# Kernel optimization log

Hardware: AMD Instinct MI355X
Metric: run time of the kernel (lower is better)

## Reference

```python
import jax, jax.numpy as jnp
import numpy as np

GROUP_SIZE = 128

def setup_inputs() -> dict:
    key = jax.random.key(0)
    k1, k2, k3, k4 = jax.random.split(key, 4)
    in_f, out_f = 4096, 4096
    num_groups = (in_f + GROUP_SIZE - 1) // GROUP_SIZE  # 32
    x = jax.random.normal(k1, (4, 2048, in_f), dtype=jnp.float32)
    qweight = jax.random.randint(k2, (out_f, in_f), 0, 16, dtype=jnp.int32)
    scales = jax.random.uniform(k3, (out_f, num_groups), dtype=jnp.float32)
    bias = jax.random.normal(k4, (out_f,), dtype=jnp.float32)
    return {"x": x, "qweight": qweight, "scales": scales, "bias": bias}

def reference(x, qweight, scales, bias):
    out_f, in_f = qweight.shape
    # group-wise dequantize: broadcast each per-group scale over its columns
    scale_full = jnp.repeat(scales, GROUP_SIZE, axis=1)[:, :in_f]  # [out, in]
    weight = qweight.astype(scales.dtype) * scale_full             # [out, in]
    # F.linear(x, weight, bias) == x @ weight.T + bias
    return jnp.einsum('bsi,oi->bso', x, weight) + bias
```

## Files before the change

### kernel.cpp

```cpp
#include <hip/hip_runtime.h>
#include <hip/hip_bf16.h>

typedef __bf16 bf16_t;
typedef __bf16 bf16x8 __attribute__((ext_vector_type(8)));
typedef float  f32x4  __attribute__((ext_vector_type(4)));

static constexpr int M_ = 8192;
static constexpr int N_ = 4096;
static constexpr int K_ = 4096;

static constexpr int BM = 256, BN = 256, BK = 64;
static constexpr int NT = K_ / BK;
static constexpr int HT_ELEMS  = 128 * 64;
static constexpr int BUF_ELEMS = 2 * HT_ELEMS;

__device__ __forceinline__ void load_lds16(const bf16_t* g, bf16_t* l) {
  __builtin_amdgcn_global_load_lds(
      (const __attribute__((address_space(1))) void*)g,
      (__attribute__((address_space(3))) void*)l,
      16, 0, 0);
}

#define MFMA16(a, b, c) __builtin_amdgcn_mfma_f32_16x16x32_bf16((a), (b), (c), 0, 0, 0)

__global__ __launch_bounds__(256) void cvt_x_kernel(const float* __restrict__ x,
                                                    bf16_t* __restrict__ xb) {
  const size_t i = ((size_t)blockIdx.x * 256 + threadIdx.x) * 8;
  const float4 f0 = *(const float4*)(x + i);
  const float4 f1 = *(const float4*)(x + i + 4);
  bf16x8 o;
  o[0] = (bf16_t)f0.x; o[1] = (bf16_t)f0.y; o[2] = (bf16_t)f0.z; o[3] = (bf16_t)f0.w;
  o[4] = (bf16_t)f1.x; o[5] = (bf16_t)f1.y; o[6] = (bf16_t)f1.z; o[7] = (bf16_t)f1.w;
  *(bf16x8*)(xb + i) = o;
}

__global__ __launch_bounds__(256) void dequant_kernel(const int* __restrict__ q,
                                                      const float* __restrict__ s,
                                                      bf16_t* __restrict__ wb) {
  const size_t base = ((size_t)blockIdx.x * 256 + threadIdx.x) * 8;
  const int o  = (int)(base >> 12);
  const int ii = (int)(base & 4095);
  const float sc = s[(o << 5) + (ii >> 7)];
  const int4 q0 = *(const int4*)(q + base);
  const int4 q1 = *(const int4*)(q + base + 4);
  bf16x8 w;
  w[0] = (bf16_t)((float)q0.x * sc); w[1] = (bf16_t)((float)q0.y * sc);
  w[2] = (bf16_t)((float)q0.z * sc); w[3] = (bf16_t)((float)q0.w * sc);
  w[4] = (bf16_t)((float)q1.x * sc); w[5] = (bf16_t)((float)q1.y * sc);
  w[6] = (bf16_t)((float)q1.z * sc); w[7] = (bf16_t)((float)q1.w * sc);
  *(bf16x8*)(wb + base) = w;
}

__global__ __launch_bounds__(512, 2) void gemm_kernel(const bf16_t* __restrict__ A,
                                                      const bf16_t* __restrict__ B,
                                                      const float* __restrict__ bias,
                                                      float* __restrict__ C) {
  __shared__ __align__(16) bf16_t As[2 * BUF_ELEMS];
  __shared__ __align__(16) bf16_t Bs[2 * BUF_ELEMS];

  const int tid  = threadIdx.x;
  const int lane = tid & 63;
  const int wave = tid >> 6;
  const int ln = lane & 15;
  const int lq = lane >> 4;
  const int wm = wave >> 2;
  const int wn = wave & 3;

  const int bid = blockIdx.x;
  const int wg  = (bid & 7) * 64 + (bid >> 3);
  const int bn  = (wg & 15) * BN;
  const int bm  = (wg >> 4) * BM;

  const int r_sub = tid >> 3;
  const int g_col = ((tid & 7) ^ (r_sub & 7)) * 8;
  const size_t a_base = (size_t)(bm + r_sub) * K_ + g_col;
  const size_t b_base = (size_t)(bn + r_sub) * K_ + g_col;
  const int lds_off = tid * 8;

  auto stageA = [&](int t, int h) {
    bf16_t* d = As + (t & 1) * BUF_ELEMS + h * HT_ELEMS + lds_off;
    const bf16_t* s = A + a_base + (size_t)(h * 128) * K_ + (size_t)t * BK;
    load_lds16(s, d);
    load_lds16(s + (size_t)64 * K_, d + 4096);
  };
  auto stageB = [&](int t, int h) {
    bf16_t* d = Bs + (t & 1) * BUF_ELEMS + h * HT_ELEMS + lds_off;
    const bf16_t* s = B + b_base + (size_t)(h * 128) * K_ + (size_t)t * BK;
    load_lds16(s, d);
    load_lds16(s + (size_t)64 * K_, d + 4096);
  };

  const int kx0 = (lq * 8) ^ ((ln & 7) * 8);
  const int kx1 = (32 + lq * 8) ^ ((ln & 7) * 8);
  const int a_row_off = (wm * 16 + ln) * 64;
  const int b_row_off = (wn * 32 + ln) * 64;

  f32x4 acc[8][4] = {};

  stageA(0, 0); stageB(0, 0); stageB(0, 1); stageA(0, 1);
  stageA(1, 0); stageB(1, 0); stageB(1, 1);
  asm volatile("s_waitcnt vmcnt(6)" ::: "memory");
  __builtin_amdgcn_s_barrier();

  for (int T = 0; T < NT; ++T) {
    const bf16_t* as = As + (T & 1) * BUF_ELEMS;
    const bf16_t* bs = Bs + (T & 1) * BUF_ELEMS;
    bf16x8 af[4][2], bqA[2][2], bqB[2][2];

#pragma unroll
    for (int i = 0; i < 4; ++i) {
      const bf16_t* p = as + a_row_off + i * 2048;
      af[i][0] = *(const bf16x8*)(p + kx0);
      af[i][1] = *(const bf16x8*)(p + kx1);
    }
#pragma unroll
    for (int j = 0; j < 2; ++j) {
      const bf16_t* p = bs + b_row_off + j * 1024;
      bqA[j][0] = *(const bf16x8*)(p + kx0);
      bqA[j][1] = *(const bf16x8*)(p + kx1);
    }
    if (T + 1 < NT) stageA(T + 1, 1);
    asm volatile("s_waitcnt lgkmcnt(8)" ::: "memory");
    __builtin_amdgcn_s_barrier();
    asm volatile("s_waitcnt lgkmcnt(0)" ::: "memory");
    __builtin_amdgcn_sched_barrier(0);
    __builtin_amdgcn_s_setprio(1);
#pragma unroll
    for (int i = 0; i < 4; ++i)
#pragma unroll
      for (int j = 0; j < 2; ++j) {
        acc[i][j] = MFMA16(af[i][0], bqA[j][0], acc[i][j]);
        acc[i][j] = MFMA16(af[i][1], bqA[j][1], acc[i][j]);
      }
    __builtin_amdgcn_s_setprio(0);
    __builtin_amdgcn_s_barrier();

#pragma unroll
    for (int j = 0; j < 2; ++j) {
      const bf16_t* p = bs + HT_ELEMS + b_row_off + j * 1024;
      bqB[j][0] = *(const bf16x8*)(p + kx0);
      bqB[j][1] = *(const bf16x8*)(p + kx1);
    }
    if (T + 2 < NT) stageA(T + 2, 0);
    __builtin_amdgcn_s_barrier();
    asm volatile("s_waitcnt lgkmcnt(0)" ::: "memory");
    __builtin_amdgcn_sched_barrier(0);
    __builtin_amdgcn_s_setprio(1);
#pragma unroll
    for (int i = 0; i < 4; ++i)
#pragma unroll
      for (int j = 0; j < 2; ++j) {
        acc[i][j + 2] = MFMA16(af[i][0], bqB[j][0], acc[i][j + 2]);
        acc[i][j + 2] = MFMA16(af[i][1], bqB[j][1], acc[i][j + 2]);
      }
    __builtin_amdgcn_s_setprio(0);
    __builtin_amdgcn_s_barrier();

#pragma unroll
    for (int i = 0; i < 4; ++i) {
      const bf16_t* p = as + HT_ELEMS + a_row_off + i * 2048;
      af[i][0] = *(const bf16x8*)(p + kx0);
      af[i][1] = *(const bf16x8*)(p + kx1);
    }
    if (T + 2 < NT) stageB(T + 2, 0);
    __builtin_amdgcn_s_barrier();
    asm volatile("s_waitcnt lgkmcnt(0)" ::: "memory");
    __builtin_amdgcn_sched_barrier(0);
    __builtin_amdgcn_s_setprio(1);
#pragma unroll
    for (int i = 0; i < 4; ++i)
#pragma unroll
      for (int j = 0; j < 2; ++j) {
        acc[i + 4][j + 2] = MFMA16(af[i][0], bqB[j][0], acc[i + 4][j + 2]);
        acc[i + 4][j + 2] = MFMA16(af[i][1], bqB[j][1], acc[i + 4][j + 2]);
      }
    __builtin_amdgcn_s_setprio(0);
    __builtin_amdgcn_s_barrier();

    if (T + 2 < NT) {
      stageB(T + 2, 1);
      asm volatile("s_waitcnt vmcnt(6)" ::: "memory");
    } else {
      asm volatile("s_waitcnt vmcnt(0)" ::: "memory");
    }
    __builtin_amdgcn_s_barrier();
    __builtin_amdgcn_sched_barrier(0);
    __builtin_amdgcn_s_setprio(1);
#pragma unroll
    for (int i = 0; i < 4; ++i)
#pragma unroll
      for (int j = 0; j < 2; ++j) {
        acc[i + 4][j] = MFMA16(af[i][0], bqA[j][0], acc[i + 4][j]);
        acc[i + 4][j] = MFMA16(af[i][1], bqA[j][1], acc[i + 4][j]);
      }
    __builtin_amdgcn_s_setprio(0);
    __builtin_amdgcn_s_barrier();
  }

#pragma unroll
  for (int j = 0; j < 4; ++j) {
    const int col = bn + (j >> 1) * 128 + wn * 32 + (j & 1) * 16 + ln;
    const float bv = bias[col];
#pragma unroll
    for (int i = 0; i < 8; ++i) {
      const int row0 = bm + (i >> 2) * 128 + (i & 3) * 32 + wm * 16 + lq * 4;
      float* cp = C + (size_t)row0 * N_ + col;
#pragma unroll
      for (int r = 0; r < 4; ++r) {
        *cp = acc[i][j][r] + bv;
        cp += N_;
      }
    }
  }
}

extern "C" void kernel_launch(void* const* d_in, const int* in_sizes, int n_in,
                              void* d_out, int out_size, void* d_ws, size_t ws_size,
                              hipStream_t stream) {
  const float* x    = (const float*)d_in[0];
  const int*   qw   = (const int*)d_in[1];
  const float* sc   = (const float*)d_in[2];
  const float* bias = (const float*)d_in[3];
  float* out = (float*)d_out;

  bf16_t* xb = (bf16_t*)d_ws;
  bf16_t* wb = xb + (size_t)M_ * K_;

  cvt_x_kernel<<<(int)(((size_t)M_ * K_) / (256 * 8)), 256, 0, stream>>>(x, xb);
  dequant_kernel<<<(int)(((size_t)N_ * K_) / (256 * 8)), 256, 0, stream>>>(qw, sc, wb);

  const int nwg = (N_ / BN) * (M_ / BM);
  gemm_kernel<<<nwg, 512, 0, stream>>>(xb, wb, bias, out);
}
```

Baseline: 491.3 us.

## Prefetch next tile's B fragments during last phase and stage epilogue through LDS

```diff
diff --git a/kernel.cpp b/kernel.cpp
--- a/kernel.cpp
+++ b/kernel.cpp
@@ -96,120 +96,160 @@
   const int b_row_off = (wn * 32 + ln) * 64;
 
   f32x4 acc[8][4] = {};
+  bf16x8 bq0[2][2], bq1[2][2];
+
+#define TILE_BODY(T_, AS_, BS_, BQC_, BQN_)                                    \
+  {                                                                            \
+    const bf16_t* as = (AS_);                                                  \
+    const bf16_t* bs = (BS_);                                                  \
+    bf16x8 af[4][2], bqB[2][2];                                                \
+               \
+    _Pragma("unroll")                                                          \
+    for (int i = 0; i < 4; ++i) {                                              \
+      const bf16_t* p = as + a_row_off + i * 2048;                             \
+      af[i][0] = *(const bf16x8*)(p + kx0);                                    \
+      af[i][1] = *(const bf16x8*)(p + kx1);                                    \
+    }                                                                          \
+    if ((T_) + 1 < NT) stageA((T_) + 1, 1);                                    \
+    asm volatile("s_waitcnt lgkmcnt(8)" ::: "memory");                         \
+    __builtin_amdgcn_s_barrier();                                              \
+    asm volatile("s_waitcnt lgkmcnt(0)" ::: "memory");                         \
+    __builtin_amdgcn_sched_barrier(0);                                         \
+    __builtin_amdgcn_s_setprio(1);                                             \
+    _Pragma("unroll")                                                          \
+    for (int i = 0; i < 4; ++i)                                                \
+      _Pragma("unroll")                                                        \
+      for (int j = 0; j < 2; ++j) {                                            \
+        acc[i][j] = MFMA16(af[i][0], BQC_[j][0], acc[i][j]);                   \
+        acc[i][j] = MFMA16(af[i][1], BQC_[j][1], acc[i][j]);                   \
+      }                                                                        \
+    __builtin_amdgcn_s_setprio(0);                                             \
+    __builtin_amdgcn_s_barrier();                                              \
+               \
+    _Pragma("unroll")                                                          \
+    for (int j = 0; j < 2; ++j) {                                              \
+      const bf16_t* p = bs + HT_ELEMS + b_row_off + j * 1024;                  \
+      bqB[j][0] = *(const bf16x8*)(p + kx0);                                   \
+      bqB[j][1] = *(const bf16x8*)(p + kx1);                                   \
+    }                                                                          \
+    if ((T_) + 2 < NT) stageA((T_) + 2, 0);                                    \
+    __builtin_amdgcn_s_barrier();                                              \
+    asm volatile("s_waitcnt lgkmcnt(0)" ::: "memory");                         \
+    __builtin_amdgcn_sched_barrier(0);                                         \
+    __builtin_amdgcn_s_setprio(1);                                             \
+    _Pragma("unroll")                                                          \
+    for (int i = 0; i < 4; ++i)                                                \
+      _Pragma("unroll")                                                        \
+      for (int j = 0; j < 2; ++j) {                                            \
+        acc[i][j + 2] = MFMA16(af[i][0], bqB[j][0], acc[i][j + 2]);            \
+        acc[i][j + 2] = MFMA16(af[i][1], bqB[j][1], acc[i][j + 2]);            \
+      }                                                                        \
+    __builtin_amdgcn_s_setprio(0);                                             \
+    __builtin_amdgcn_s_barrier();                                              \
+     \
+    _Pragma("unroll")                                                          \
+    for (int i = 0; i < 4; ++i) {                                              \
+      const bf16_t* p = as + HT_ELEMS + a_row_off + i * 2048;                  \
+      af[i][0] = *(const bf16x8*)(p + kx0);                                    \
+      af[i][1] = *(const bf16x8*)(p + kx1);                                    \
+    }                                                                          \
+    if ((T_) + 2 < NT) stageB((T_) + 2, 0);                                    \
+    __builtin_amdgcn_s_barrier();                                              \
+    asm volatile("s_waitcnt lgkmcnt(0)" ::: "memory");                         \
+    __builtin_amdgcn_sched_barrier(0);                                         \
+    __builtin_amdgcn_s_setprio(1);                                             \
+    _Pragma("unroll")                                                          \
+    for (int i = 0; i < 4; ++i)                                                \
+      _Pragma("unroll")                                                        \
+      for (int j = 0; j < 2; ++j) {                                            \
+        acc[i + 4][j + 2] = MFMA16(af[i][0], bqB[j][0], acc[i + 4][j + 2]);    \
+        acc[i + 4][j + 2] = MFMA16(af[i][1], bqB[j][1], acc[i + 4][j + 2]);    \
+      }                                                                        \
+    __builtin_amdgcn_s_setprio(0);                                             \
+    __builtin_amdgcn_s_barrier();                                              \
+                                                         \
+    if ((T_) + 2 < NT) {                                                       \
+      stageB((T_) + 2, 1);                                                     \
+      asm volatile("s_waitcnt vmcnt(6)" ::: "memory");                         \
+    } else {                                                                   \
+      asm volatile("s_waitcnt vmcnt(0)" ::: "memory");                         \
+    }                                                                          \
+    __builtin_amdgcn_s_barrier();                                              \
+    if ((T_) + 1 < NT) {                                                       \
+      const bf16_t* nbs = ((T_) + 1) & 1 ? Bs + BUF_ELEMS : Bs;                \
+      _Pragma("unroll")                                                        \
+      for (int j = 0; j < 2; ++j) {                                            \
+        const bf16_t* p = nbs + b_row_off + j * 1024;                          \
+        BQN_[j][0] = *(const bf16x8*)(p + kx0);                                \
+        BQN_[j][1] = *(const bf16x8*)(p + kx1);                                \
+      }                                                                        \
+    }                                                                          \
+    __builtin_amdgcn_sched_barrier(0);                                         \
+    __builtin_amdgcn_s_setprio(1);                                             \
+    _Pragma("unroll")                                                          \
+    for (int i = 0; i < 4; ++i)                                                \
+      _Pragma("unroll")                                                        \
+      for (int j = 0; j < 2; ++j) {                                            \
+        acc[i + 4][j] = MFMA16(af[i][0], BQC_[j][0], acc[i + 4][j]);           \
+        acc[i + 4][j] = MFMA16(af[i][1], BQC_[j][1], acc[i + 4][j]);           \
+      }                                                                        \
+    __builtin_amdgcn_s_setprio(0);                                             \
+    __builtin_amdgcn_s_barrier();                                              \
+  }
 
   stageA(0, 0); stageB(0, 0); stageB(0, 1); stageA(0, 1);
   stageA(1, 0); stageB(1, 0); stageB(1, 1);
   asm volatile("s_waitcnt vmcnt(6)" ::: "memory");
   __builtin_amdgcn_s_barrier();
-
-  for (int T = 0; T < NT; ++T) {
-    const bf16_t* as = As + (T & 1) * BUF_ELEMS;
-    const bf16_t* bs = Bs + (T & 1) * BUF_ELEMS;
-    bf16x8 af[4][2], bqA[2][2], bqB[2][2];
-
-#pragma unroll
-    for (int i = 0; i < 4; ++i) {
-      const bf16_t* p = as + a_row_off + i * 2048;
-      af[i][0] = *(const bf16x8*)(p + kx0);
-      af[i][1] = *(const bf16x8*)(p + kx1);
+#pragma unroll
+  for (int j = 0; j < 2; ++j) {
+    const bf16_t* p = Bs + b_row_off + j * 1024;
+    bq0[j][0] = *(const bf16x8*)(p + kx0);
+    bq0[j][1] = *(const bf16x8*)(p + kx1);
+  }
+
+  for (int T = 0; T < NT; T += 2) {
+    TILE_BODY(T,     As,             Bs,             bq0, bq1)
+    TILE_BODY(T + 1, As + BUF_ELEMS, Bs + BUF_ELEMS, bq1, bq0)
+  }
+#undef TILE_BODY
+
+  float bv[4];
+#pragma unroll
+  for (int j = 0; j < 4; ++j)
+    bv[j] = bias[bn + (j >> 1) * 128 + wn * 32 + (j & 1) * 16 + ln];
+
+  float* lds_f = (float*)As;
+  const int cb = wn * 32 + ln;
+#pragma unroll
+  for (int c = 0; c < 4; ++c) {
+#pragma unroll
+    for (int ih = 0; ih < 2; ++ih) {
+      const int i = 2 * c + ih;
+      const int rbase = ih * 32 + wm * 16 + lq * 4;
+#pragma unroll
+      for (int j = 0; j < 4; ++j) {
+        const int cl = (j >> 1) * 128 + (j & 1) * 16 + cb;
+#pragma unroll
+        for (int r = 0; r < 4; ++r) {
+          const int rl = rbase + r;
+          const int pc = cl ^ (((rl >> 2) & 1) << 4);
+          lds_f[rl * 256 + pc] = acc[i][j][r] + bv[j];
+        }
+      }
     }
-#pragma unroll
-    for (int j = 0; j < 2; ++j) {
-      const bf16_t* p = bs + b_row_off + j * 1024;
-      bqA[j][0] = *(const bf16x8*)(p + kx0);
-      bqA[j][1] = *(const bf16x8*)(p + kx1);
+    asm volatile("s_waitcnt lgkmcnt(0)" ::: "memory");
+    __builtin_amdgcn_s_barrier();
+#pragma unroll
+    for (int k = 0; k < 8; ++k) {
+      const int rr = k * 8 + wave;
+      const int pc = (lane * 4) ^ (((rr >> 2) & 1) << 4);
+      const float4 v = *(const float4*)(lds_f + rr * 256 + pc);
+      *(float4*)(C + (size_t)(bm + c * 64 + rr) * N_ + bn + lane * 4) = v;
     }
-    if (T + 1 < NT) stageA(T + 1, 1);
-    asm volatile("s_waitcnt lgkmcnt(8)" ::: "memory");
-    __builtin_amdgcn_s_barrier();
-    asm volatile("s_waitcnt lgkmcnt(0)" ::: "memory");
-    __builtin_amdgcn_sched_barrier(0);
-    __builtin_amdgcn_s_setprio(1);
-#pragma unroll
-    for (int i = 0; i < 4; ++i)
-#pragma unroll
-      for (int j = 0; j < 2; ++j) {
-        acc[i][j] = MFMA16(af[i][0], bqA[j][0], acc[i][j]);
-        acc[i][j] = MFMA16(af[i][1], bqA[j][1], acc[i][j]);
-      }
-    __builtin_amdgcn_s_setprio(0);
-    __builtin_amdgcn_s_barrier();
-
-#pragma unroll
-    for (int j = 0; j < 2; ++j) {
-      const bf16_t* p = bs + HT_ELEMS + b_row_off + j * 1024;
-      bqB[j][0] = *(const bf16x8*)(p + kx0);
-      bqB[j][1] = *(const bf16x8*)(p + kx1);
-    }
-    if (T + 2 < NT) stageA(T + 2, 0);
-    __builtin_amdgcn_s_barrier();
-    asm volatile("s_waitcnt lgkmcnt(0)" ::: "memory");
-    __builtin_amdgcn_sched_barrier(0);
-    __builtin_amdgcn_s_setprio(1);
-#pragma unroll
-    for (int i = 0; i < 4; ++i)
-#pragma unroll
-      for (int j = 0; j < 2; ++j) {
-        acc[i][j + 2] = MFMA16(af[i][0], bqB[j][0], acc[i][j + 2]);
-        acc[i][j + 2] = MFMA16(af[i][1], bqB[j][1], acc[i][j + 2]);
-      }
-    __builtin_amdgcn_s_setprio(0);
-    __builtin_amdgcn_s_barrier();
-
-#pragma unroll
-    for (int i = 0; i < 4; ++i) {
-      const bf16_t* p = as + HT_ELEMS + a_row_off + i * 2048;
-      af[i][0] = *(const bf16x8*)(p + kx0);
-      af[i][1] = *(const bf16x8*)(p + kx1);
-    }
-    if (T + 2 < NT) stageB(T + 2, 0);
-    __builtin_amdgcn_s_barrier();
-    asm volatile("s_waitcnt lgkmcnt(0)" ::: "memory");
-    __builtin_amdgcn_sched_barrier(0);
-    __builtin_amdgcn_s_setprio(1);
-#pragma unroll
-    for (int i = 0; i < 4; ++i)
-#pragma unroll
-      for (int j = 0; j < 2; ++j) {
-        acc[i + 4][j + 2] = MFMA16(af[i][0], bqB[j][0], acc[i + 4][j + 2]);
-        acc[i + 4][j + 2] = MFMA16(af[i][1], bqB[j][1], acc[i + 4][j + 2]);
-      }
-    __builtin_amdgcn_s_setprio(0);
-    __builtin_amdgcn_s_barrier();
-
-    if (T + 2 < NT) {
-      stageB(T + 2, 1);
-      asm volatile("s_waitcnt vmcnt(6)" ::: "memory");
-    } else {
-      asm volatile("s_waitcnt vmcnt(0)" ::: "memory");
-    }
-    __builtin_amdgcn_s_barrier();
-    __builtin_amdgcn_sched_barrier(0);
-    __builtin_amdgcn_s_setprio(1);
-#pragma unroll
-    for (int i = 0; i < 4; ++i)
-#pragma unroll
-      for (int j = 0; j < 2; ++j) {
-        acc[i + 4][j] = MFMA16(af[i][0], bqA[j][0], acc[i + 4][j]);
-        acc[i + 4][j] = MFMA16(af[i][1], bqA[j][1], acc[i + 4][j]);
-      }
-    __builtin_amdgcn_s_setprio(0);
-    __builtin_amdgcn_s_barrier();
-  }
-
-#pragma unroll
-  for (int j = 0; j < 4; ++j) {
-    const int col = bn + (j >> 1) * 128 + wn * 32 + (j & 1) * 16 + ln;
-    const float bv = bias[col];
-#pragma unroll
-    for (int i = 0; i < 8; ++i) {
-      const int row0 = bm + (i >> 2) * 128 + (i & 3) * 32 + wm * 16 + lq * 4;
-      float* cp = C + (size_t)row0 * N_ + col;
-#pragma unroll
-      for (int r = 0; r < 4; ++r) {
-        *cp = acc[i][j][r] + bv;
-        cp += N_;
-      }
+    if (c < 3) {
+      asm volatile("s_waitcnt lgkmcnt(0)" ::: "memory");
+      __builtin_amdgcn_s_barrier();
     }
   }
 }
```

New measurement: 511.5 us. 1.04x slower.
